# Optimization experiments

Measured on AMD Instinct MI355X. Metric: run time of the kernel, lower is better.

The kernel has to match this reference:

```python
import jax, jax.numpy as jnp
import numpy as np

N, E = 50000, 800000
IN, HID, OUT = 128, 128, 64
BN_EPS = 1e-5


def _w(key, fan_in, fan_out):
    return jax.random.normal(key, (fan_in, fan_out), dtype=jnp.float32) / np.sqrt(fan_in)


def setup_inputs() -> dict:
    key = jax.random.key(0)
    ks = jax.random.split(key, 12)
    x = jax.random.normal(ks[0], (N, IN), dtype=jnp.float32)
    src = jax.random.randint(ks[1], (E,), 0, N, dtype=jnp.int32)
    dst = jax.random.randint(ks[2], (E,), 0, N, dtype=jnp.int32)
    eps = jax.random.normal(ks[3], (N, OUT), dtype=jnp.float32)
    return {
        "x": x, "src": src, "dst": dst, "eps": eps,
        # SAGEConv 1: in -> hidden (lin_l has bias, lin_r no bias, mean aggr)
        "W1l": _w(ks[4], IN, HID), "W1r": _w(ks[5], IN, HID), "b1": jnp.zeros((HID,), jnp.float32),
        "g1": jnp.ones((HID,), jnp.float32), "be1": jnp.zeros((HID,), jnp.float32),
        # SAGEConv 2: hidden -> 2*hidden
        "W2l": _w(ks[6], HID, 2 * HID), "W2r": _w(ks[7], HID, 2 * HID), "b2": jnp.zeros((2 * HID,), jnp.float32),
        "g2": jnp.ones((2 * HID,), jnp.float32), "be2": jnp.zeros((2 * HID,), jnp.float32),
        # SAGEConv 3: 2*hidden -> 2*out
        "W3l": _w(ks[8], 2 * HID, 2 * OUT), "W3r": _w(ks[9], 2 * HID, 2 * OUT), "b3": jnp.zeros((2 * OUT,), jnp.float32),
    }


def _sage(h, src, dst, Wl, Wr, b):
    # mean-aggregate source features at destination nodes, then two GEMMs
    msg = jax.ops.segment_sum(h[src], dst, num_segments=N)          # [N, F]
    deg = jax.ops.segment_sum(jnp.ones((src.shape[0],), h.dtype), dst, num_segments=N)
    aggr = msg / jnp.maximum(deg, 1.0)[:, None]
    return aggr @ Wl + h @ Wr + b


def _bn(h, gamma, beta):
    m = jnp.mean(h, axis=0)
    v = jnp.var(h, axis=0)
    return gamma * (h - m) * jax.lax.rsqrt(v + BN_EPS) + beta


def reference(x, src, dst, eps, W1l, W1r, b1, g1, be1, W2l, W2r, b2, g2, be2, W3l, W3r, b3):
    h = jax.nn.relu(_sage(x, src, dst, W1l, W1r, b1))
    h = _bn(h, g1, be1)                       # dropout = identity (eval)
    h = jax.nn.relu(_sage(h, src, dst, W2l, W2r, b2))
    h = _bn(h, g2, be2)
    h = _sage(h, src, dst, W3l, W3r, b3)      # [N, 2*OUT]
    mean, log_std = jnp.split(h, 2, axis=-1)
    z = mean + jnp.exp(log_std) * eps         # reparameterize
    return z
```

## Files before the change

### kernel.cpp

```cpp
#include <hip/hip_runtime.h>
#include <math.h>

#define N_NODES 50000
#define N_EDGES 800000
#define BN_EPS_F 1e-5f
#define SCAN_BS 512
#define SCAN_NB 98
#define GXR 196
#define GXP2 200

typedef unsigned short ushort_t;
typedef unsigned int uint_t;
typedef __attribute__((ext_vector_type(8))) short bf16x8;
typedef __attribute__((ext_vector_type(4))) float f32x4;

static __device__ __forceinline__ float4 ld4(const float* p) {
    return *reinterpret_cast<const float4*>(p);
}
static __device__ __forceinline__ float bf2f(ushort_t u) {
    return __uint_as_float(((uint_t)u) << 16);
}
static __device__ __forceinline__ ushort_t f2b(float f) {
    uint_t u = __float_as_uint(f);
    u += 0x7fffu + ((u >> 16) & 1u);
    return (ushort_t)(u >> 16);
}


__global__ void k_zero_i32(int* __restrict__ p, int n) {
    int i = blockIdx.x * blockDim.x + threadIdx.x;
    if (i < n) p[i] = 0;
}

__global__ void k_pre(const int* __restrict__ dst, int* __restrict__ deg,
                      ushort_t* __restrict__ rank,
                      const float* __restrict__ x, ushort_t* __restrict__ xb,
                      const float* __restrict__ W1l, const float* __restrict__ W1r,
                      const float* __restrict__ W2l, ushort_t* __restrict__ wt1l,
                      ushort_t* __restrict__ wt1r, ushort_t* __restrict__ wt2l) {
    int b = blockIdx.x;
    if (b < 6250) {
        int role = b & 1;
        int id = (b >> 1) * 256 + threadIdx.x;
        if (role == 0) {
            rank[id] = (ushort_t)atomicAdd(&deg[dst[id]], 1);
        } else {
            float4 a = ld4(x + (size_t)id * 8);
            float4 c = ld4(x + (size_t)id * 8 + 4);
            uint_t o0 = (uint_t)f2b(a.x) | ((uint_t)f2b(a.y) << 16);
            uint_t o1 = (uint_t)f2b(a.z) | ((uint_t)f2b(a.w) << 16);
            uint_t o2 = (uint_t)f2b(c.x) | ((uint_t)f2b(c.y) << 16);
            uint_t o3 = (uint_t)f2b(c.z) | ((uint_t)f2b(c.w) << 16);
            *reinterpret_cast<uint4*>(xb + (size_t)id * 8) = make_uint4(o0, o1, o2, o3);
        }
    } else {
        int idx = (b - 6250) * 256 + threadIdx.x;
        if (idx < 16384) {
            int f = idx >> 7, k = idx & 127;
            wt1l[idx] = f2b(W1l[(size_t)k * 128 + f]);
        } else if (idx < 32768) {
            int j = idx - 16384;
            int f = j >> 7, k = j & 127;
            wt1r[j] = f2b(W1r[(size_t)k * 128 + f]);
        } else {
            int j = idx - 32768;
            int f = j >> 7, k = j & 127;
            wt2l[j] = f2b(W2l[(size_t)k * 256 + f]);
        }
    }
}

__global__ void k_scan1(const int* __restrict__ deg, int* __restrict__ offs, int* __restrict__ bsum) {
    __shared__ int sh[SCAN_BS];
    int t = threadIdx.x;
    int g = blockIdx.x * SCAN_BS + t;
    int v = (g < N_NODES) ? deg[g] : 0;
    sh[t] = v;
    __syncthreads();
    for (int off = 1; off < SCAN_BS; off <<= 1) {
        int add = (t >= off) ? sh[t - off] : 0;
        __syncthreads();
        sh[t] += add;
        __syncthreads();
    }
    if (g < N_NODES) offs[g] = sh[t] - v;
    if (t == SCAN_BS - 1) bsum[blockIdx.x] = sh[t];
}

__global__ void k_scan2(int* __restrict__ bsum, int nb) {
    __shared__ int sh[128];
    int t = threadIdx.x;
    int v = (t < nb) ? bsum[t] : 0;
    sh[t] = v;
    __syncthreads();
    for (int off = 1; off < 128; off <<= 1) {
        int add = (t >= off) ? sh[t - off] : 0;
        __syncthreads();
        sh[t] += add;
        __syncthreads();
    }
    if (t < nb) bsum[t] = sh[t] - v;
}

__global__ void k_scan3(const int* __restrict__ deg, int* __restrict__ offs,
                        const int* __restrict__ bsum, float* __restrict__ inv_deg) {
    int g = blockIdx.x * blockDim.x + threadIdx.x;
    if (g < N_NODES) {
        offs[g] += bsum[g / SCAN_BS];
        int d = deg[g];
        inv_deg[g] = 1.0f / (float)(d > 1 ? d : 1);
    }
}

__global__ void k_fill2(const int* __restrict__ src, const int* __restrict__ dst,
                        const int* __restrict__ offs, const ushort_t* __restrict__ rank,
                        ushort_t* __restrict__ eids) {
    int e = blockIdx.x * blockDim.x + threadIdx.x;
    if (e < N_EDGES) eids[offs[dst[e]] + (int)rank[e]] = (ushort_t)src[e];
}


__global__ void k_prep2(const float* __restrict__ W2r, const float* __restrict__ b2,
                        const float* __restrict__ scsh1, ushort_t* __restrict__ wt2r,
                        float* __restrict__ bias2) {
    int bid = blockIdx.x;
    if (bid < 128) {
        int idx = bid * 256 + threadIdx.x;
        int f = idx >> 7, k = idx & 127;
        wt2r[idx] = f2b(scsh1[k] * W2r[(size_t)k * 256 + f]);
    } else {
        int f = threadIdx.x;
        float s = b2[f];
        for (int k = 0; k < 128; ++k) s += scsh1[128 + k] * W2r[(size_t)k * 256 + f];
        bias2[f] = s;
    }
}

__global__ void k_prep3(const float* __restrict__ W3l, const float* __restrict__ W3r,
                        const float* __restrict__ b3, const float* __restrict__ scsh2,
                        ushort_t* __restrict__ wt3l, ushort_t* __restrict__ wt3r,
                        float* __restrict__ bias3l, float* __restrict__ bias3r) {
    int bid = blockIdx.x;
    if (bid < 256) {
        int half = bid >> 7;
        int idx = (bid & 127) * 256 + threadIdx.x;
        int f = idx >> 8, k = idx & 255;
        const float* W = half ? W3r : W3l;
        ushort_t* WT = half ? wt3r : wt3l;
        WT[idx] = f2b(scsh2[k] * W[(size_t)k * 128 + f]);
    } else {
        int t = threadIdx.x;
        int f = t & 127;
        const float* W = (t < 128) ? W3l : W3r;
        float s = (t < 128) ? 0.f : b3[f];
        for (int k = 0; k < 256; ++k) s += scsh2[256 + k] * W[(size_t)k * 128 + f];
        float* out = (t < 128) ? bias3l : bias3r;
        out[f] = s;
    }
}


#define ACCUM8(a) do { \
    acc[0] += bf2f((ushort_t)(a).x); acc[1] += bf2f((ushort_t)((a).x >> 16)); \
    acc[2] += bf2f((ushort_t)(a).y); acc[3] += bf2f((ushort_t)((a).y >> 16)); \
    acc[4] += bf2f((ushort_t)(a).z); acc[5] += bf2f((ushort_t)((a).z >> 16)); \
    acc[6] += bf2f((ushort_t)(a).w); acc[7] += bf2f((ushort_t)((a).w >> 16)); } while (0)

static __device__ __forceinline__ void gather_rows_g(
        const ushort_t* __restrict__ h, const ushort_t* __restrict__ eids,
        int beg, int d, size_t coff, float* acc) {
    int j = 0;
    for (; j + 8 <= d; j += 8) {
        uint4 a[8];
#pragma unroll
        for (int k = 0; k < 8; ++k) {
            int s = eids[beg + j + k];
            a[k] = *reinterpret_cast<const uint4*>(h + (size_t)s * 128 + coff);
        }
#pragma unroll
        for (int k = 0; k < 8; ++k) ACCUM8(a[k]);
    }
    for (; j + 4 <= d; j += 4) {
        uint4 a[4];
#pragma unroll
        for (int k = 0; k < 4; ++k) {
            int s = eids[beg + j + k];
            a[k] = *reinterpret_cast<const uint4*>(h + (size_t)s * 128 + coff);
        }
#pragma unroll
        for (int k = 0; k < 4; ++k) ACCUM8(a[k]);
    }
    for (; j + 2 <= d; j += 2) {
        int s0 = eids[beg + j];
        int s1 = eids[beg + j + 1];
        uint4 a = *reinterpret_cast<const uint4*>(h + (size_t)s0 * 128 + coff);
        uint4 b = *reinterpret_cast<const uint4*>(h + (size_t)s1 * 128 + coff);
        ACCUM8(a); ACCUM8(b);
    }
    if (j < d) {
        int s0 = eids[beg + j];
        uint4 a = *reinterpret_cast<const uint4*>(h + (size_t)s0 * 128 + coff);
        ACCUM8(a);
    }
}

template<int BN>
__global__ __launch_bounds__(256) void k_agg16(
        const ushort_t* __restrict__ h, const ushort_t* __restrict__ eids,
        const int* __restrict__ offs, const int* __restrict__ deg,
        const float* __restrict__ inv_deg, const float* __restrict__ scsh,
        ushort_t* __restrict__ out) {
    const int node = blockIdx.x * 16 + (threadIdx.x >> 4);
    const int lr = threadIdx.x & 15;
    if (node >= N_NODES) return;
    float acc[8];
#pragma unroll
    for (int v = 0; v < 8; ++v) acc[v] = 0.f;
    const int beg = offs[node];
    const int d = deg[node];
    const size_t coff = (size_t)lr * 8;
    gather_rows_g(h, eids, beg, d, coff, acc);

    float sc = inv_deg[node];
    if (BN) {
        float4 sa0 = ld4(&scsh[lr * 8]), sa1 = ld4(&scsh[lr * 8 + 4]);
        float4 sb0 = ld4(&scsh[128 + lr * 8]), sb1 = ld4(&scsh[128 + lr * 8 + 4]);
        if (d > 0) {
            acc[0] = acc[0] * sc * sa0.x + sb0.x; acc[1] = acc[1] * sc * sa0.y + sb0.y;
            acc[2] = acc[2] * sc * sa0.z + sb0.z; acc[3] = acc[3] * sc * sa0.w + sb0.w;
            acc[4] = acc[4] * sc * sa1.x + sb1.x; acc[5] = acc[5] * sc * sa1.y + sb1.y;
            acc[6] = acc[6] * sc * sa1.z + sb1.z; acc[7] = acc[7] * sc * sa1.w + sb1.w;
        } else {
#pragma unroll
            for (int v = 0; v < 8; ++v) acc[v] = 0.f;
        }
    } else {
#pragma unroll
        for (int v = 0; v < 8; ++v) acc[v] *= sc;
    }
    uint4 o;
    o.x = (uint_t)f2b(acc[0]) | ((uint_t)f2b(acc[1]) << 16);
    o.y = (uint_t)f2b(acc[2]) | ((uint_t)f2b(acc[3]) << 16);
    o.z = (uint_t)f2b(acc[4]) | ((uint_t)f2b(acc[5]) << 16);
    o.w = (uint_t)f2b(acc[6]) | ((uint_t)f2b(acc[7]) << 16);
    *reinterpret_cast<uint4*>(out + (size_t)node * 128 + coff) = o;
}

__global__ __launch_bounds__(256) void k_agg_reparam(
        const ushort_t* __restrict__ t3, const ushort_t* __restrict__ eids,
        const int* __restrict__ offs, const int* __restrict__ deg,
        const float* __restrict__ inv_deg, const ushort_t* __restrict__ u,
        const float* __restrict__ eps, float* __restrict__ z) {
    const int node = blockIdx.x * 16 + (threadIdx.x >> 4);
    const int lr = threadIdx.x & 15;
    if (node >= N_NODES) return;
    float acc[8];
#pragma unroll
    for (int v = 0; v < 8; ++v) acc[v] = 0.f;
    const int beg = offs[node];
    const int d = deg[node];
    const size_t coff = (size_t)lr * 8;
    gather_rows_g(t3, eids, beg, d, coff, acc);
    float ls[8];
#pragma unroll
    for (int v = 0; v < 8; ++v) ls[v] = __shfl_down(acc[v], 8);

    if (lr < 8) {
        float sc = inv_deg[node];
        uint4 um4 = *reinterpret_cast<const uint4*>(u + (size_t)node * 128 + lr * 8);
        uint4 ul4 = *reinterpret_cast<const uint4*>(u + (size_t)node * 128 + 64 + lr * 8);
        const float* ep = eps + (size_t)node * 64 + lr * 8;
        float4 e0 = ld4(ep), e1 = ld4(ep + 4);
        float um[8], ul[8];
        um[0] = bf2f((ushort_t)um4.x); um[1] = bf2f((ushort_t)(um4.x >> 16));
        um[2] = bf2f((ushort_t)um4.y); um[3] = bf2f((ushort_t)(um4.y >> 16));
        um[4] = bf2f((ushort_t)um4.z); um[5] = bf2f((ushort_t)(um4.z >> 16));
        um[6] = bf2f((ushort_t)um4.w); um[7] = bf2f((ushort_t)(um4.w >> 16));
        ul[0] = bf2f((ushort_t)ul4.x); ul[1] = bf2f((ushort_t)(ul4.x >> 16));
        ul[2] = bf2f((ushort_t)ul4.y); ul[3] = bf2f((ushort_t)(ul4.y >> 16));
        ul[4] = bf2f((ushort_t)ul4.z); ul[5] = bf2f((ushort_t)(ul4.z >> 16));
        ul[6] = bf2f((ushort_t)ul4.w); ul[7] = bf2f((ushort_t)(ul4.w >> 16));
        float4 o0, o1;
        o0.x = (acc[0] * sc + um[0]) + expf(ls[0] * sc + ul[0]) * e0.x;
        o0.y = (acc[1] * sc + um[1]) + expf(ls[1] * sc + ul[1]) * e0.y;
        o0.z = (acc[2] * sc + um[2]) + expf(ls[2] * sc + ul[2]) * e0.z;
        o0.w = (acc[3] * sc + um[3]) + expf(ls[3] * sc + ul[3]) * e0.w;
        o1.x = (acc[4] * sc + um[4]) + expf(ls[4] * sc + ul[4]) * e1.x;
        o1.y = (acc[5] * sc + um[5]) + expf(ls[5] * sc + ul[5]) * e1.y;
        o1.z = (acc[6] * sc + um[6]) + expf(ls[6] * sc + ul[6]) * e1.z;
        o1.w = (acc[7] * sc + um[7]) + expf(ls[7] * sc + ul[7]) * e1.w;
        float* zp = z + (size_t)node * 64 + lr * 8;
        *reinterpret_cast<float4*>(zp) = o0;
        *reinterpret_cast<float4*>(zp + 4) = o1;
    }
}


template<int RELU, int DUAL, int STATS, int SEL3, int K, int YT>
__global__ __launch_bounds__(256) void k_gemm_direct(
        const ushort_t* __restrict__ A1, const ushort_t* __restrict__ A2,
        const ushort_t* __restrict__ B1, const ushort_t* __restrict__ B2,
        const float* __restrict__ bias, ushort_t* __restrict__ out,
        int F, float* __restrict__ partials,
        const float* __restrict__ bias2, ushort_t* __restrict__ out2) {
    const int bid = blockIdx.x;
    const int grp = bid >> 3;
    const int y = grp / 25;
    const int rq = grp - y * 25;
    const int r = (bid & 7) + (rq << 3);
    if (r >= GXR) return;
    const int row0 = r * 256;

    int colblk = y, outsel = 0;
    if (SEL3) { colblk = y & 1; outsel = y >> 1; }
    const int col0 = colblk * 64;
    const ushort_t* __restrict__ Bp = (SEL3 && outsel) ? B2 : B1;
    const float* __restrict__ biasp = (SEL3 && outsel) ? bias2 : bias;
    ushort_t* __restrict__ outp = (SEL3 && outsel) ? out2 : out;

    const int tid = threadIdx.x;
    const int lane = tid & 63;
    const int w = tid >> 6;
    const int q = lane >> 4, lr = lane & 15;
    const int wrow = row0 + w * 64;

    int arow[4];
    const ushort_t* bptr[4];
#pragma unroll
    for (int f = 0; f < 4; ++f) {
        int rr = wrow + f * 16 + lr;
        arow[f] = rr < N_NODES ? rr : N_NODES - 1;
        bptr[f] = Bp + (size_t)(col0 + f * 16 + lr) * K + q * 8;
    }

    f32x4 acc[4][4];
#pragma unroll
    for (int mf = 0; mf < 4; ++mf)
#pragma unroll
        for (int nf = 0; nf < 4; ++nf)
            acc[mf][nf] = (f32x4){0.f, 0.f, 0.f, 0.f};

#pragma unroll
    for (int m = 0; m < (DUAL ? 2 : 1); ++m) {
        const ushort_t* __restrict__ A = m ? A2 : A1;
        const ushort_t* __restrict__ B = m ? B2 : Bp;
#pragma unroll
        for (int k0 = 0; k0 < K; k0 += 32) {
            bf16x8 av[4], bv[4];
#pragma unroll
            for (int f = 0; f < 4; ++f) {
                av[f] = *reinterpret_cast<const bf16x8*>(A + (size_t)arow[f] * K + k0 + q * 8);
                bv[f] = SEL3 ? *reinterpret_cast<const bf16x8*>(bptr[f] + k0)
                             : *reinterpret_cast<const bf16x8*>(B + (size_t)(col0 + f * 16 + lr) * K + k0 + q * 8);
            }
#pragma unroll
            for (int mf = 0; mf < 4; ++mf)
#pragma unroll
                for (int nf = 0; nf < 4; ++nf)
                    acc[mf][nf] = __builtin_amdgcn_mfma_f32_16x16x32_bf16(
                        av[mf], bv[nf], acc[mf][nf], 0, 0, 0);
        }
    }

    __shared__ __align__(16) short lw[4][64][68];
    __shared__ float sdf[2][16][64];

    float s[4], s2[4];
#pragma unroll
    for (int nf = 0; nf < 4; ++nf) { s[nf] = 0.f; s2[nf] = 0.f; }
#pragma unroll
    for (int nf = 0; nf < 4; ++nf) {
        float bvs = biasp[col0 + nf * 16 + lr];
#pragma unroll
        for (int mf = 0; mf < 4; ++mf) {
#pragma unroll
            for (int b = 0; b < 4; ++b) {
                int rrow = mf * 16 + q * 4 + b;
                float v = acc[mf][nf][b] + bvs;
                if (RELU) v = fmaxf(v, 0.f);
                if (STATS && (wrow + rrow) < N_NODES) { s[nf] += v; s2[nf] += v * v; }
                lw[w][rrow][nf * 16 + lr] = (short)f2b(v);
            }
        }
    }
#pragma unroll
    for (int rr = 0; rr < 8; ++rr) {
        int row = rr * 8 + (lane >> 3);
        int gr = wrow + row;
        if (gr < N_NODES) {
            uint4 vv = *reinterpret_cast<const uint4*>(&lw[w][row][(lane & 7) * 8]);
            *reinterpret_cast<uint4*>(outp + (size_t)gr * F + col0 + (lane & 7) * 8) = vv;
        }
    }

    if constexpr (STATS) {
        const int u = w * 4 + q;
#pragma unroll
        for (int nf = 0; nf < 4; ++nf) {
            sdf[0][u][nf * 16 + lr] = s[nf];
            sdf[1][u][nf * 16 + lr] = s2[nf];
        }
        __syncthreads();
        if (tid < 64) {
            float ss = 0.f, qq = 0.f;
#pragma unroll
            for (int u2 = 0; u2 < 16; ++u2) {
                ss += sdf[0][u2][tid];
                qq += sdf[1][u2][tid];
            }
            int cg = col0 + tid;
            partials[(size_t)cg * GXP2 + r] = ss;
            partials[(size_t)(F + cg) * GXP2 + r] = qq;
        }
    }
}


template<int F>
__global__ __launch_bounds__(64) void k_bn_scsh(
        const float* __restrict__ partials, const float* __restrict__ gamma,
        const float* __restrict__ beta, float* __restrict__ scsh) {
    const int c = blockIdx.x;
    const int l = threadIdx.x;
    float s = 0.f, q2 = 0.f;
    for (int g = l; g < GXR; g += 64) {
        s += partials[(size_t)c * GXP2 + g];
        q2 += partials[(size_t)(F + c) * GXP2 + g];
    }
#pragma unroll
    for (int off = 1; off < 64; off <<= 1) {
        s += __shfl_xor(s, off);
        q2 += __shfl_xor(q2, off);
    }
    if (l == 0) {
        float mean = s * (1.0f / N_NODES);
        float var = q2 * (1.0f / N_NODES) - mean * mean;
        float sc = gamma[c] * rsqrtf(var + BN_EPS_F);
        scsh[c] = sc;
        scsh[F + c] = beta[c] - mean * sc;
    }
}


extern "C" void kernel_launch(void* const* d_in, const int* in_sizes, int n_in,
                              void* d_out, int out_size, void* d_ws, size_t ws_size,
                              hipStream_t stream) {
    (void)in_sizes; (void)n_in; (void)out_size; (void)ws_size;
    const float* x   = (const float*)d_in[0];
    const int*   src = (const int*)d_in[1];
    const int*   dst = (const int*)d_in[2];
    const float* eps = (const float*)d_in[3];
    const float* W1l = (const float*)d_in[4];
    const float* W1r = (const float*)d_in[5];
    const float* b1  = (const float*)d_in[6];
    const float* g1  = (const float*)d_in[7];
    const float* be1 = (const float*)d_in[8];
    const float* W2l = (const float*)d_in[9];
    const float* W2r = (const float*)d_in[10];
    const float* b2  = (const float*)d_in[11];
    const float* g2  = (const float*)d_in[12];
    const float* be2 = (const float*)d_in[13];
    const float* W3l = (const float*)d_in[14];
    const float* W3r = (const float*)d_in[15];
    const float* b3  = (const float*)d_in[16];
    float* z = (float*)d_out;

    char* ws = (char*)d_ws;
    size_t off = 0;
    auto alloc = [&](size_t bytes) -> char* {
        char* p = ws + off;
        off += (bytes + 255) & ~(size_t)255;
        return p;
    };
    int*      deg    = (int*)alloc(N_NODES * 4);
    size_t zero_bytes = off;
    ushort_t* rank   = (ushort_t*)alloc((size_t)N_EDGES * 2);
    ushort_t* eids   = (ushort_t*)alloc((size_t)N_EDGES * 2);
    float*    scshs  = (float*)alloc(1024 * 4);
    float*    biases = (float*)alloc(512 * 4);
    int*      offs   = (int*)alloc(N_NODES * 4);
    int*      bsum   = (int*)alloc(128 * 4);
    float*    invd   = (float*)alloc(N_NODES * 4);
    ushort_t* xb     = (ushort_t*)alloc((size_t)N_NODES * 128 * 2);
    ushort_t* h1b    = (ushort_t*)alloc((size_t)N_NODES * 128 * 2);
    ushort_t* h2b    = (ushort_t*)alloc((size_t)N_NODES * 256 * 2);
    ushort_t* aggrb  = (ushort_t*)alloc((size_t)N_NODES * 256 * 2);
    ushort_t* u3b    = (ushort_t*)alloc((size_t)N_NODES * 128 * 2);
    float*    parts  = (float*)alloc((size_t)512 * GXP2 * 4);
    ushort_t* wt1l   = (ushort_t*)alloc(128 * 128 * 2);
    ushort_t* wt1r   = (ushort_t*)alloc(128 * 128 * 2);
    ushort_t* wt2l   = (ushort_t*)alloc(256 * 128 * 2);
    ushort_t* wt2r   = (ushort_t*)alloc(256 * 128 * 2);
    ushort_t* wt3l   = (ushort_t*)alloc(128 * 256 * 2);
    ushort_t* wt3r   = (ushort_t*)alloc(128 * 256 * 2);
    ushort_t* t3b    = aggrb;

    float* scsh1  = scshs;
    float* scsh2  = scshs + 256;
    float* bias2  = biases;
    float* bias3l = biases + 256;
    float* bias3r = biases + 384;

    k_zero_i32<<<((int)(zero_bytes / 4) + 255) / 256, 256, 0, stream>>>((int*)ws, (int)(zero_bytes / 4));
    k_pre<<<6506, 256, 0, stream>>>(dst, deg, rank, x, xb, W1l, W1r, W2l, wt1l, wt1r, wt2l);
    k_scan1<<<SCAN_NB, SCAN_BS, 0, stream>>>(deg, offs, bsum);
    k_scan2<<<1, 128, 0, stream>>>(bsum, SCAN_NB);
    k_scan3<<<(N_NODES + 255) / 256, 256, 0, stream>>>(deg, offs, bsum, invd);
    k_fill2<<<(N_EDGES + 255) / 256, 256, 0, stream>>>(src, dst, offs, rank, eids);

    const int AGG_BLKS = N_NODES / 16;

    k_agg16<0><<<AGG_BLKS, 256, 0, stream>>>(xb, eids, offs, deg, invd, nullptr, aggrb);
    k_gemm_direct<1, 1, 1, 0, 128, 2><<<400, 256, 0, stream>>>(
        aggrb, xb, wt1l, wt1r, b1, h1b, 128, parts, nullptr, nullptr);
    k_bn_scsh<128><<<128, 64, 0, stream>>>(parts, g1, be1, scsh1);

    k_prep2<<<129, 256, 0, stream>>>(W2r, b2, scsh1, wt2r, bias2);
    k_agg16<1><<<AGG_BLKS, 256, 0, stream>>>(h1b, eids, offs, deg, invd, scsh1, aggrb);
    k_gemm_direct<1, 1, 1, 0, 128, 4><<<800, 256, 0, stream>>>(
        aggrb, h1b, wt2l, wt2r, bias2, h2b, 256, parts, nullptr, nullptr);
    k_bn_scsh<256><<<256, 64, 0, stream>>>(parts, g2, be2, scsh2);

    k_prep3<<<257, 256, 0, stream>>>(W3l, W3r, b3, scsh2, wt3l, wt3r, bias3l, bias3r);
    k_gemm_direct<0, 0, 0, 1, 256, 4><<<800, 256, 0, stream>>>(
        h2b, nullptr, wt3l, wt3r, bias3l, t3b, 128, nullptr, bias3r, u3b);
    k_agg_reparam<<<AGG_BLKS, 256, 0, stream>>>(t3b, eids, offs, deg, invd, u3b, eps, z);
}
```

Measured before the change: 256.3 us.

## Halve GEMM row tile to 128 and pad degree counters to reduce atomic contention

Each GEMM block now covers 128 rows instead of 256, with two M-fragments per wave instead of four. This doubles the grid size to improve occupancy and CU coverage across the three GEMMs, at the cost of reloading B fragments more often. Separately, the per-node degree counters are padded to a 64-byte stride so the histogram atomics hit distinct cache lines, and a compact degree array is written during the scan for later kernels. The padding adds 3.2 MB of zeroing and strided reads in the scan kernels.

```diff
diff --git a/kernel.cpp b/kernel.cpp
--- a/kernel.cpp
+++ b/kernel.cpp
@@ -6,8 +6,9 @@
 #define BN_EPS_F 1e-5f
 #define SCAN_BS 512
 #define SCAN_NB 98
-#define GXR 196
-#define GXP2 200
+#define RC 391
+#define RQ 49
+#define GXP2 392
 
 typedef unsigned short ushort_t;
 typedef unsigned int uint_t;
@@ -32,7 +33,7 @@
     if (i < n) p[i] = 0;
 }
 
-__global__ void k_pre(const int* __restrict__ dst, int* __restrict__ deg,
+__global__ void k_pre(const int* __restrict__ dst, int* __restrict__ deg2,
                       ushort_t* __restrict__ rank,
                       const float* __restrict__ x, ushort_t* __restrict__ xb,
                       const float* __restrict__ W1l, const float* __restrict__ W1r,
@@ -43,7 +44,7 @@
         int role = b & 1;
         int id = (b >> 1) * 256 + threadIdx.x;
         if (role == 0) {
-            rank[id] = (ushort_t)atomicAdd(&deg[dst[id]], 1);
+            rank[id] = (ushort_t)atomicAdd(&deg2[dst[id] * 16], 1);
         } else {
             float4 a = ld4(x + (size_t)id * 8);
             float4 c = ld4(x + (size_t)id * 8 + 4);
@@ -70,11 +71,11 @@
     }
 }
 
-__global__ void k_scan1(const int* __restrict__ deg, int* __restrict__ offs, int* __restrict__ bsum) {
+__global__ void k_scan1(const int* __restrict__ deg2, int* __restrict__ offs, int* __restrict__ bsum) {
     __shared__ int sh[SCAN_BS];
     int t = threadIdx.x;
     int g = blockIdx.x * SCAN_BS + t;
-    int v = (g < N_NODES) ? deg[g] : 0;
+    int v = (g < N_NODES) ? deg2[g * 16] : 0;
     sh[t] = v;
     __syncthreads();
     for (int off = 1; off < SCAN_BS; off <<= 1) {
@@ -102,12 +103,14 @@
     if (t < nb) bsum[t] = sh[t] - v;
 }
 
-__global__ void k_scan3(const int* __restrict__ deg, int* __restrict__ offs,
-                        const int* __restrict__ bsum, float* __restrict__ inv_deg) {
+__global__ void k_scan3(const int* __restrict__ deg2, int* __restrict__ offs,
+                        const int* __restrict__ bsum, float* __restrict__ inv_deg,
+                        int* __restrict__ degc) {
     int g = blockIdx.x * blockDim.x + threadIdx.x;
     if (g < N_NODES) {
         offs[g] += bsum[g / SCAN_BS];
-        int d = deg[g];
+        int d = deg2[g * 16];
+        degc[g] = d;
         inv_deg[g] = 1.0f / (float)(d > 1 ? d : 1);
     }
 }
@@ -296,7 +299,7 @@
 }
 
 
-template<int RELU, int DUAL, int STATS, int SEL3, int K, int YT>
+template<int RELU, int DUAL, int STATS, int SEL3, int K>
 __global__ __launch_bounds__(256) void k_gemm_direct(
         const ushort_t* __restrict__ A1, const ushort_t* __restrict__ A2,
         const ushort_t* __restrict__ B1, const ushort_t* __restrict__ B2,
@@ -304,12 +307,13 @@
         int F, float* __restrict__ partials,
         const float* __restrict__ bias2, ushort_t* __restrict__ out2) {
     const int bid = blockIdx.x;
-    const int grp = bid >> 3;
-    const int y = grp / 25;
-    const int rq = grp - y * 25;
-    const int r = (bid & 7) + (rq << 3);
-    if (r >= GXR) return;
-    const int row0 = r * 256;
+    const int c = bid & 7;
+    const int g2 = bid >> 3;
+    const int y = g2 / RQ;
+    const int rq = g2 - y * RQ;
+    const int r = rq * 8 + c;
+    if (r >= RC) return;
+    const int row0 = r * 128;
 
     int colblk = y, outsel = 0;
     if (SEL3) { colblk = y & 1; outsel = y >> 1; }
@@ -322,20 +326,18 @@
     const int lane = tid & 63;
     const int w = tid >> 6;
     const int q = lane >> 4, lr = lane & 15;
-    const int wrow = row0 + w * 64;
-
-    int arow[4];
-    const ushort_t* bptr[4];
-#pragma unroll
-    for (int f = 0; f < 4; ++f) {
-        int rr = wrow + f * 16 + lr;
-        arow[f] = rr < N_NODES ? rr : N_NODES - 1;
-        bptr[f] = Bp + (size_t)(col0 + f * 16 + lr) * K + q * 8;
-    }
-
-    f32x4 acc[4][4];
-#pragma unroll
-    for (int mf = 0; mf < 4; ++mf)
+    const int wrow = row0 + w * 32;
+
+    int arow[2];
+#pragma unroll
+    for (int mf = 0; mf < 2; ++mf) {
+        int rr = wrow + mf * 16 + lr;
+        arow[mf] = rr < N_NODES ? rr : N_NODES - 1;
+    }
+
+    f32x4 acc[2][4];
+#pragma unroll
+    for (int mf = 0; mf < 2; ++mf)
 #pragma unroll
         for (int nf = 0; nf < 4; ++nf)
             acc[mf][nf] = (f32x4){0.f, 0.f, 0.f, 0.f};
@@ -346,15 +348,15 @@
         const ushort_t* __restrict__ B = m ? B2 : Bp;
 #pragma unroll
         for (int k0 = 0; k0 < K; k0 += 32) {
-            bf16x8 av[4], bv[4];
-#pragma unroll
-            for (int f = 0; f < 4; ++f) {
-                av[f] = *reinterpret_cast<const bf16x8*>(A + (size_t)arow[f] * K + k0 + q * 8);
-                bv[f] = SEL3 ? *reinterpret_cast<const bf16x8*>(bptr[f] + k0)
-                             : *reinterpret_cast<const bf16x8*>(B + (size_t)(col0 + f * 16 + lr) * K + k0 + q * 8);
-            }
-#pragma unroll
-            for (int mf = 0; mf < 4; ++mf)
+            bf16x8 av[2], bv[4];
+#pragma unroll
+            for (int mf = 0; mf < 2; ++mf)
+                av[mf] = *reinterpret_cast<const bf16x8*>(A + (size_t)arow[mf] * K + k0 + q * 8);
+#pragma unroll
+            for (int nf = 0; nf < 4; ++nf)
+                bv[nf] = *reinterpret_cast<const bf16x8*>(B + (size_t)(col0 + nf * 16 + lr) * K + k0 + q * 8);
+#pragma unroll
+            for (int mf = 0; mf < 2; ++mf)
 #pragma unroll
                 for (int nf = 0; nf < 4; ++nf)
                     acc[mf][nf] = __builtin_amdgcn_mfma_f32_16x16x32_bf16(
@@ -362,7 +364,7 @@
         }
     }
 
-    __shared__ __align__(16) short lw[4][64][68];
+    __shared__ __align__(16) short lw[4][32][68];
     __shared__ float sdf[2][16][64];
 
     float s[4], s2[4];
@@ -372,7 +374,7 @@
     for (int nf = 0; nf < 4; ++nf) {
         float bvs = biasp[col0 + nf * 16 + lr];
 #pragma unroll
-        for (int mf = 0; mf < 4; ++mf) {
+        for (int mf = 0; mf < 2; ++mf) {
 #pragma unroll
             for (int b = 0; b < 4; ++b) {
                 int rrow = mf * 16 + q * 4 + b;
@@ -384,7 +386,7 @@
         }
     }
 #pragma unroll
-    for (int rr = 0; rr < 8; ++rr) {
+    for (int rr = 0; rr < 4; ++rr) {
         int row = rr * 8 + (lane >> 3);
         int gr = wrow + row;
         if (gr < N_NODES) {
@@ -423,7 +425,7 @@
     const int c = blockIdx.x;
     const int l = threadIdx.x;
     float s = 0.f, q2 = 0.f;
-    for (int g = l; g < GXR; g += 64) {
+    for (int g = l; g < RC; g += 64) {
         s += partials[(size_t)c * GXP2 + g];
         q2 += partials[(size_t)(F + c) * GXP2 + g];
     }
@@ -472,7 +474,7 @@
         off += (bytes + 255) & ~(size_t)255;
         return p;
     };
-    int*      deg    = (int*)alloc(N_NODES * 4);
+    int*      deg2   = (int*)alloc((size_t)N_NODES * 16 * 4);
     size_t zero_bytes = off;
     ushort_t* rank   = (ushort_t*)alloc((size_t)N_EDGES * 2);
     ushort_t* eids   = (ushort_t*)alloc((size_t)N_EDGES * 2);
@@ -480,6 +482,7 @@
     float*    biases = (float*)alloc(512 * 4);
     int*      offs   = (int*)alloc(N_NODES * 4);
     int*      bsum   = (int*)alloc(128 * 4);
+    int*      degc   = (int*)alloc(N_NODES * 4);
     float*    invd   = (float*)alloc(N_NODES * 4);
     ushort_t* xb     = (ushort_t*)alloc((size_t)N_NODES * 128 * 2);
     ushort_t* h1b    = (ushort_t*)alloc((size_t)N_NODES * 128 * 2);
@@ -502,27 +505,27 @@
     float* bias3r = biases + 384;
 
     k_zero_i32<<<((int)(zero_bytes / 4) + 255) / 256, 256, 0, stream>>>((int*)ws, (int)(zero_bytes / 4));
-    k_pre<<<6506, 256, 0, stream>>>(dst, deg, rank, x, xb, W1l, W1r, W2l, wt1l, wt1r, wt2l);
-    k_scan1<<<SCAN_NB, SCAN_BS, 0, stream>>>(deg, offs, bsum);
+    k_pre<<<6506, 256, 0, stream>>>(dst, deg2, rank, x, xb, W1l, W1r, W2l, wt1l, wt1r, wt2l);
+    k_scan1<<<SCAN_NB, SCAN_BS, 0, stream>>>(deg2, offs, bsum);
     k_scan2<<<1, 128, 0, stream>>>(bsum, SCAN_NB);
-    k_scan3<<<(N_NODES + 255) / 256, 256, 0, stream>>>(deg, offs, bsum, invd);
+    k_scan3<<<(N_NODES + 255) / 256, 256, 0, stream>>>(deg2, offs, bsum, invd, degc);
     k_fill2<<<(N_EDGES + 255) / 256, 256, 0, stream>>>(src, dst, offs, rank, eids);
 
     const int AGG_BLKS = N_NODES / 16;
 
-    k_agg16<0><<<AGG_BLKS, 256, 0, stream>>>(xb, eids, offs, deg, invd, nullptr, aggrb);
-    k_gemm_direct<1, 1, 1, 0, 128, 2><<<400, 256, 0, stream>>>(
+    k_agg16<0><<<AGG_BLKS, 256, 0, stream>>>(xb, eids, offs, degc, invd, nullptr, aggrb);
+    k_gemm_direct<1, 1, 1, 0, 128><<<8 * RQ * 2, 256, 0, stream>>>(
         aggrb, xb, wt1l, wt1r, b1, h1b, 128, parts, nullptr, nullptr);
     k_bn_scsh<128><<<128, 64, 0, stream>>>(parts, g1, be1, scsh1);
 
     k_prep2<<<129, 256, 0, stream>>>(W2r, b2, scsh1, wt2r, bias2);
-    k_agg16<1><<<AGG_BLKS, 256, 0, stream>>>(h1b, eids, offs, deg, invd, scsh1, aggrb);
-    k_gemm_direct<1, 1, 1, 0, 128, 4><<<800, 256, 0, stream>>>(
+    k_agg16<1><<<AGG_BLKS, 256, 0, stream>>>(h1b, eids, offs, degc, invd, scsh1, aggrb);
+    k_gemm_direct<1, 1, 1, 0, 128><<<8 * RQ * 4, 256, 0, stream>>>(
         aggrb, h1b, wt2l, wt2r, bias2, h2b, 256, parts, nullptr, nullptr);
     k_bn_scsh<256><<<256, 64, 0, stream>>>(parts, g2, be2, scsh2);
 
     k_prep3<<<257, 256, 0, stream>>>(W3l, W3r, b3, scsh2, wt3l, wt3r, bias3l, bias3r);
-    k_gemm_direct<0, 0, 0, 1, 256, 4><<<800, 256, 0, stream>>>(
+    k_gemm_direct<0, 0, 0, 1, 256><<<8 * RQ * 4, 256, 0, stream>>>(
         h2b, nullptr, wt3l, wt3r, bias3l, t3b, 128, nullptr, bias3r, u3b);
-    k_agg_reparam<<<AGG_BLKS, 256, 0, stream>>>(t3b, eids, offs, deg, invd, u3b, eps, z);
-}
+    k_agg_reparam<<<AGG_BLKS, 256, 0, stream>>>(t3b, eids, offs, degc, invd, u3b, eps, z);
+}
```

Measured after the change: 278.4 us. 1.09x slower.
